# Performance work log

Measured on AMD Instinct MI355X. Metric: run time of the kernel, lower is better.

The kernel has to match this reference:

```python
import jax, jax.numpy as jnp
import numpy as np
from math import sqrt

THRESHOLD = 0.5
NEG_POS_RATIO = 3
ALPHA = 1.0


def make_priors():
    fms = [(38, 0.1, [1.0, 2.0, 0.5]), (19, 0.2, [1.0, 2.0, 0.5, 3.0, 1.0 / 3]),
           (10, 0.375, [1.0, 2.0, 0.5, 3.0, 1.0 / 3]), (5, 0.55, [1.0, 2.0, 0.5, 3.0, 1.0 / 3]),
           (3, 0.725, [1.0, 2.0, 0.5]), (1, 0.9, [1.0, 2.0, 0.5])]
    scales = [0.1, 0.2, 0.375, 0.55, 0.725, 0.9]
    priors = []
    for k, (d, s, ratios) in enumerate(fms):
        for i in range(d):
            for j in range(d):
                cx = (i + 0.5) / d
                cy = (j + 0.5) / d
                for r in ratios:
                    priors.append([cx, cy, s * sqrt(r), s / sqrt(r)])
                    if r == 1.0:
                        add = sqrt(scales[k] * scales[k + 1]) if k + 1 < len(scales) else 1.0
                        priors.append([cx, cy, add, add])
    return np.clip(np.asarray(priors, dtype=np.float32), 0.0, 1.0)  # [8732, 4]


def cxcy_to_xy(b):
    return jnp.concatenate([b[..., :2] - b[..., 2:] / 2.0, b[..., :2] + b[..., 2:] / 2.0], -1)


def jaccard(a, b):
    # a: [O,4] cxcy, b: [P,4] cxcy -> IoU [O,P]
    a_xy, b_xy = cxcy_to_xy(a), cxcy_to_xy(b)
    lt = jnp.maximum(a_xy[:, None, :2], b_xy[None, :, :2])
    rb = jnp.minimum(a_xy[:, None, 2:], b_xy[None, :, 2:])
    wh = jnp.clip(rb - lt, 0.0)
    inter = wh[..., 0] * wh[..., 1]
    area_a = (a_xy[:, 2] - a_xy[:, 0]) * (a_xy[:, 3] - a_xy[:, 1])
    area_b = (b_xy[:, 2] - b_xy[:, 0]) * (b_xy[:, 3] - b_xy[:, 1])
    return inter / (area_a[:, None] + area_b[None, :] - inter)


def cxcy_to_gcxgcy(cxcy, priors):
    g_cxcy = (cxcy[..., :2] - priors[..., :2]) / (priors[..., 2:] / 10.0)
    g_wh = jnp.log(cxcy[..., 2:] / priors[..., 2:]) * 5.0
    return jnp.concatenate([g_cxcy, g_wh], -1)


def match_one(boxes_i, priors):
    # boxes_i: [O,4] cxcy
    n_obj = boxes_i.shape[0]
    ov = jaccard(boxes_i, priors)                      # [O, P]
    ov_per_prior = ov.max(0)                           # [P]
    obj_per_prior = ov.argmax(0)                       # [P]
    prior_per_obj = ov.argmax(1)                       # [O]
    obj_per_prior = obj_per_prior.at[prior_per_obj].set(jnp.arange(n_obj))
    ov_per_prior = ov_per_prior.at[prior_per_obj].set(1.0)
    labels = (ov_per_prior >= THRESHOLD).astype(jnp.int32)  # [P], 1=text 0=bg
    true_locs = cxcy_to_gcxgcy(boxes_i[obj_per_prior], priors)  # [P,4]
    return labels, true_locs


def setup_inputs() -> dict:
    key = jax.random.key(0)
    k1, k2, k3, k4 = jax.random.split(key, 4)
    priors = jnp.asarray(make_priors())
    B, P, O = 512, priors.shape[0], 16
    predicted_locs = jax.random.normal(k1, (B, P, 4), dtype=jnp.float32)
    predicted_scores = jax.random.normal(k2, (B, P, 2), dtype=jnp.float32)
    centers = 0.2 + 0.6 * jax.random.uniform(k3, (B, O, 2), dtype=jnp.float32)
    wh = 0.05 + 0.35 * jax.random.uniform(k4, (B, O, 2), dtype=jnp.float32)
    boxes = jnp.concatenate([centers, wh], -1)  # cxcy format
    return {"predicted_locs": predicted_locs, "predicted_scores": predicted_scores,
            "boxes": boxes, "priors": priors}


def reference(predicted_locs, predicted_scores, boxes, priors):
    B, P, _ = predicted_locs.shape
    labels, true_locs = jax.vmap(match_one, in_axes=(0, None))(boxes, priors)  # [B,P], [B,P,4]
    pos = labels != 0
    mask = pos.astype(predicted_locs.dtype)            # [B,P]
    n_pos = pos.sum(1)                                 # [B]

    # localization L1 loss (mean over positive box coordinates)
    loc_abs = jnp.abs(predicted_locs - true_locs).sum(-1)  # [B,P]
    loc_loss = (loc_abs * mask).sum() / (mask.sum() * 4.0)

    # per-prior cross-entropy
    logp = jax.nn.log_softmax(predicted_scores, -1)
    ce = -jnp.take_along_axis(logp, labels[..., None], -1)[..., 0]  # [B,P]

    conf_pos = (ce * mask).sum()
    ce_neg = jnp.where(pos, 0.0, ce)
    ce_neg = jnp.sort(ce_neg, axis=1)[:, ::-1]         # descending
    hard = jnp.arange(P)[None, :] < (NEG_POS_RATIO * n_pos)[:, None]
    conf_hn = (ce_neg * hard.astype(ce_neg.dtype)).sum()
    conf_loss = (conf_pos + conf_hn) / n_pos.sum().astype(predicted_locs.dtype)
    return conf_loss + ALPHA * loc_loss
```

## Files before the change

kernel.cpp:

```cpp
#include <hip/hip_runtime.h>

#define NP 8732
#define NQ (NP / 4)
#define NPT 35
#define NO 16
#define BLK 256
#define NWAVE (BLK / 64)
#define SPLIT 4
#define CHUNK (NP / SPLIT)


__global__ __launch_bounds__(BLK, 8) void match_kernel(
    const float* __restrict__ boxes,
    const float* __restrict__ priors,
    unsigned char* __restrict__ g_obj,
    float* __restrict__ g_bv,
    int*   __restrict__ g_bi)
{
    const int b    = blockIdx.x;
    const int s    = blockIdx.y;
    const int tid  = threadIdx.x;
    const int lane = tid & 63;
    const int wv   = tid >> 6;
    const int quad = tid & 3;
    const int objLo = quad << 2;
    const int lo = s * CHUNK, hi = lo + CHUNK;

    __shared__ float s_bxy[NO][4];
    __shared__ float s_barea[NO];
    __shared__ float s_redv[NO * NWAVE];
    __shared__ int   s_redi[NO * NWAVE];

    if (tid < NO) {
        const float* bx = boxes + (size_t)b * NO * 4 + tid * 4;
        float cx = bx[0], cy = bx[1], w = bx[2], h = bx[3];
        s_bxy[tid][0] = cx - w * 0.5f; s_bxy[tid][1] = cy - h * 0.5f;
        s_bxy[tid][2] = cx + w * 0.5f; s_bxy[tid][3] = cy + h * 0.5f;
        s_barea[tid] = w * h;
    }
    __syncthreads();

    float rx0[4], ry0[4], rx1[4], ry1[4], ra[4];
#pragma unroll
    for (int j = 0; j < 4; j++) {
        rx0[j] = s_bxy[objLo + j][0]; ry0[j] = s_bxy[objLo + j][1];
        rx1[j] = s_bxy[objLo + j][2]; ry1[j] = s_bxy[objLo + j][3];
        ra[j]  = s_barea[objLo + j];
    }

    float tbv[4]; int tbp[4];
#pragma unroll
    for (int j = 0; j < 4; j++) { tbv[j] = -1.0f; tbp[j] = lo; }

    unsigned char* obj_row = g_obj + (size_t)b * NP;
    for (int p = lo + (tid >> 2); p < hi; p += (BLK / 4)) {
        float4 pr = ((const float4*)priors)[p];
        float px0 = pr.x - pr.z * 0.5f, py0 = pr.y - pr.w * 0.5f;
        float px1 = pr.x + pr.z * 0.5f, py1 = pr.y + pr.w * 0.5f;
        float areab = pr.z * pr.w;
        float bv = -1.0f; int bo = objLo;
#pragma unroll
        for (int j = 0; j < 4; j++) {
            float ix0 = fmaxf(rx0[j], px0);
            float iy0 = fmaxf(ry0[j], py0);
            float ix1 = fminf(rx1[j], px1);
            float iy1 = fminf(ry1[j], py1);
            float iw = fmaxf(ix1 - ix0, 0.0f);
            float ih = fmaxf(iy1 - iy0, 0.0f);
            float inter = iw * ih;
            float den = ra[j] + areab - inter;
            float iou = inter * __builtin_amdgcn_rcpf(den);
            if (iou > bv)     { bv = iou; bo = objLo + j; }
            if (iou > tbv[j]) { tbv[j] = iou; tbp[j] = p; }
        }
        float vN = __shfl_xor(bv, 1, 64);
        int   oN = __shfl_xor(bo, 1, 64);
        bool take = (quad & 1) ? (vN >= bv) : (vN > bv);
        if (take) { bv = vN; bo = oN; }
        vN = __shfl_xor(bv, 2, 64);
        oN = __shfl_xor(bo, 2, 64);
        take = (quad & 2) ? (vN >= bv) : (vN > bv);
        if (take) { bv = vN; bo = oN; }
        if (quad == 0) {
            bool pos = (bv >= 0.5f);
            obj_row[p] = (unsigned char)(bo | (pos ? 0x80 : 0));
        }
    }

#pragma unroll
    for (int j = 0; j < 4; j++) {
        float v = tbv[j]; int i = tbp[j];
        for (int off = 32; off >= 4; off >>= 1) {
            float v2 = __shfl_down(v, off, 64);
            int   i2 = __shfl_down(i, off, 64);
            if (v2 > v || (v2 == v && i2 < i)) { v = v2; i = i2; }
        }
        if (lane < 4) {
            s_redv[(objLo + j) * NWAVE + wv] = v;
            s_redi[(objLo + j) * NWAVE + wv] = i;
        }
    }
    __syncthreads();
    if (tid < NO) {
        float v = s_redv[tid * NWAVE]; int i = s_redi[tid * NWAVE];
#pragma unroll
        for (int w = 1; w < NWAVE; w++) {
            float v2 = s_redv[tid * NWAVE + w]; int i2 = s_redi[tid * NWAVE + w];
            if (v2 > v || (v2 == v && i2 < i)) { v = v2; i = i2; }
        }
        g_bv[((size_t)b * NO + tid) * SPLIT + s] = v;
        g_bi[((size_t)b * NO + tid) * SPLIT + s] = i;
    }
}

__device__ __forceinline__ int hist_select(unsigned* hist, unsigned* s_part,
                                           unsigned* s_csuf, unsigned* s_sel,
                                           unsigned& kk, int tid, int lane, int wv)
{
    unsigned ps = 0;
#pragma unroll
    for (int i = 0; i < 16; i++) ps += hist[tid * 16 + i];
    s_part[tid] = ps;
    __syncthreads();
    if (wv == 0) {
        unsigned c0 = s_part[4 * lane + 0], c1 = s_part[4 * lane + 1];
        unsigned c2 = s_part[4 * lane + 2], c3 = s_part[4 * lane + 3];
        unsigned g = c0 + c1 + c2 + c3;
        unsigned incl = g;
#pragma unroll
        for (int off = 1; off < 64; off <<= 1) {
            unsigned o = __shfl_down(incl, off, 64);
            if (lane + off < 64) incl += o;
        }
        unsigned excl = incl - g;
        s_csuf[4 * lane + 3] = excl;
        s_csuf[4 * lane + 2] = excl + c3;
        s_csuf[4 * lane + 1] = excl + c3 + c2;
        s_csuf[4 * lane + 0] = excl + c3 + c2 + c1;
    }
    __syncthreads();
    unsigned base = s_csuf[tid];
    if (base < kk && kk <= base + s_part[tid]) {
        unsigned run = base;
        for (int i = 15; i >= 0; i--) {
            unsigned h = hist[tid * 16 + i];
            if (kk <= run + h) { s_sel[0] = (unsigned)(tid * 16 + i); s_sel[1] = kk - run; break; }
            run += h;
        }
    }
    __syncthreads();
    kk = s_sel[1];
    return (int)s_sel[0];
}

__global__ __launch_bounds__(BLK, 2) void loss_kernel(
    const float* __restrict__ plocs,
    const float* __restrict__ pscores,
    const float* __restrict__ boxes,
    const float* __restrict__ priors,
    const unsigned char* __restrict__ g_obj,
    const float* __restrict__ g_bv,
    const int*   __restrict__ g_bi,
    float* __restrict__ loc_out,
    float* __restrict__ conf_out,
    int*   __restrict__ npos_out)
{
    const int b    = blockIdx.x;
    const int tid  = threadIdx.x;
    const int lane = tid & 63;
    const int wv   = tid >> 6;

    __shared__ unsigned char s_obj[NP];
    __shared__ unsigned s_hist[4096];
    __shared__ unsigned s_part[256];
    __shared__ unsigned s_csuf[256];
    __shared__ unsigned s_sel[2];
    __shared__ float s_bcw[NO][4];
    __shared__ int   s_bestp[NO];
    __shared__ float s_tval;
    __shared__ float s_fred[3 * NWAVE];
    __shared__ int   s_ired[NWAVE];

    const unsigned* objw = (const unsigned*)(g_obj + (size_t)b * NP);
    for (int i = tid; i < NP / 4; i += BLK) ((unsigned*)s_obj)[i] = objw[i];
    if (tid < NO * 4) ((float*)s_bcw)[tid] = boxes[(size_t)b * NO * 4 + tid];
    if (tid < NO) {
        const float* bv = g_bv + ((size_t)b * NO + tid) * SPLIT;
        const int*   bi = g_bi + ((size_t)b * NO + tid) * SPLIT;
        float v = bv[0]; int i = bi[0];
#pragma unroll
        for (int s = 1; s < SPLIT; s++) {
            float v2 = bv[s]; int i2 = bi[s];
            if (v2 > v || (v2 == v && i2 < i)) { v = v2; i = i2; }
        }
        s_bestp[tid] = i;
    }
    __syncthreads();
    if (tid == 0) {
#pragma unroll
        for (int o = 0; o < NO; o++) s_obj[s_bestp[o]] = (unsigned char)(0x80 | o);
    }
    __syncthreads();

    float ce[NPT];
    float loc_sum = 0.0f, conf_pos = 0.0f; int np = 0;
    const float2* sc2 = (const float2*)(pscores + (size_t)b * NP * 2);
    const float4* pl4 = (const float4*)(plocs  + (size_t)b * NP * 4);
#pragma unroll
    for (int k = 0; k < NPT; k++) {
        int p = tid + k * BLK;
        float v = 0.0f;
        if (p < NP) {
            unsigned m = s_obj[p];
            bool pos = (m & 0x80) != 0;
            float2 s = sc2[p];
            float mx = fmaxf(s.x, s.y);
            float dd = fabsf(s.x - s.y);
            float cev = mx + __logf(1.0f + __expf(-dd)) - (pos ? s.y : s.x);
            if (pos) {
                np++;
                conf_pos += cev;
                int o = m & 15;
                float4 pr = ((const float4*)priors)[p];
                float gx = (s_bcw[o][0] - pr.x) / (pr.z / 10.0f);
                float gy = (s_bcw[o][1] - pr.y) / (pr.w / 10.0f);
                float gw = __logf(s_bcw[o][2] / pr.z) * 5.0f;
                float gh = __logf(s_bcw[o][3] / pr.w) * 5.0f;
                float4 pl = pl4[p];
                loc_sum += fabsf(pl.x - gx) + fabsf(pl.y - gy)
                         + fabsf(pl.z - gw) + fabsf(pl.w - gh);
            } else {
                v = cev;
            }
        }
        ce[k] = v;
    }

    int npw = np;
    for (int off = 32; off; off >>= 1) npw += __shfl_down(npw, off, 64);
    if (lane == 0) s_ired[wv] = npw;
    __syncthreads();
    int n_pos = 0;
#pragma unroll
    for (int w = 0; w < NWAVE; w++) n_pos += s_ired[w];

    const int K = 3 * n_pos;
    const bool selAll = (K >= NP);
    float t = 0.0f;
    if (!selAll) {
        unsigned kk = (unsigned)K;
        for (int i = tid; i < 4096; i += BLK) s_hist[i] = 0u;
        __syncthreads();
#pragma unroll
        for (int k = 0; k < NPT; k++)
            atomicAdd(&s_hist[__float_as_uint(ce[k]) >> 19], 1u);
        __syncthreads();
        unsigned b1 = (unsigned)hist_select(s_hist, s_part, s_csuf, s_sel, kk, tid, lane, wv);
        unsigned cnt1 = s_hist[b1];
        if (cnt1 == 1u) {
#pragma unroll
            for (int k = 0; k < NPT; k++)
                if ((__float_as_uint(ce[k]) >> 19) == b1) s_tval = ce[k];
            __syncthreads();
            t = s_tval;
        } else {
            __syncthreads();
            for (int i = tid; i < 4096; i += BLK) s_hist[i] = 0u;
            __syncthreads();
#pragma unroll
            for (int k = 0; k < NPT; k++) {
                unsigned u = __float_as_uint(ce[k]);
                if ((u >> 19) == b1) atomicAdd(&s_hist[(u >> 7) & 0xFFFu], 1u);
            }
            __syncthreads();
            unsigned b2 = (unsigned)hist_select(s_hist, s_part, s_csuf, s_sel, kk, tid, lane, wv);
            unsigned p2 = (b1 << 12) | b2;
            unsigned cnt2 = s_hist[b2];
            if (cnt2 == 1u) {
#pragma unroll
                for (int k = 0; k < NPT; k++)
                    if ((__float_as_uint(ce[k]) >> 7) == p2) s_tval = ce[k];
                __syncthreads();
                t = s_tval;
            } else {
                __syncthreads();
                for (int i = tid; i < 4096; i += BLK) s_hist[i] = 0u;
                __syncthreads();
#pragma unroll
                for (int k = 0; k < NPT; k++) {
                    unsigned u = __float_as_uint(ce[k]);
                    if ((u >> 7) == p2) atomicAdd(&s_hist[u & 0x7Fu], 1u);
                }
                __syncthreads();
                unsigned b3 = (unsigned)hist_select(s_hist, s_part, s_csuf, s_sel, kk, tid, lane, wv);
                t = __uint_as_float((p2 << 7) | b3);
            }
        }
    }

    float sgt = 0.0f; int cgt = 0;
#pragma unroll
    for (int k = 0; k < NPT; k++) {
        float v = ce[k];
        if (selAll || v > t) { sgt += v; cgt++; }
    }

    float a = sgt, c = conf_pos, l = loc_sum; int g = cgt;
    for (int off = 32; off; off >>= 1) {
        a += __shfl_down(a, off, 64);
        c += __shfl_down(c, off, 64);
        l += __shfl_down(l, off, 64);
        g += __shfl_down(g, off, 64);
    }
    __syncthreads();
    if (lane == 0) {
        s_fred[wv] = a; s_fred[NWAVE + wv] = c; s_fred[2 * NWAVE + wv] = l;
        s_ired[wv] = g;
    }
    __syncthreads();
    if (tid == 0) {
        float sa = 0.0f, sc = 0.0f, sl = 0.0f; int sg = 0;
#pragma unroll
        for (int w = 0; w < NWAVE; w++) {
            sa += s_fred[w]; sc += s_fred[NWAVE + w]; sl += s_fred[2 * NWAVE + w];
            sg += s_ired[w];
        }
        float conf_hn = selAll ? sa : (sa + (float)(K - sg) * t);
        conf_out[b] = sc + conf_hn;
        loc_out[b]  = sl;
        npos_out[b] = n_pos;
    }
}

__global__ __launch_bounds__(BLK, 2) void mbox_row_kernel(
    const float* __restrict__ plocs, const float* __restrict__ pscores,
    const float* __restrict__ boxes, const float* __restrict__ priors,
    float* __restrict__ loc_out, float* __restrict__ conf_out,
    int* __restrict__ npos_out)
{
    const int b = blockIdx.x, tid = threadIdx.x, lane = tid & 63, wv = tid >> 6;
    const int par = tid & 1, objLo = par << 3;
    __shared__ __align__(16) float s_ce[NP];
    __shared__ unsigned char s_obj[NP];
    __shared__ float s_bcw[NO][4], s_bxy[NO][4], s_barea[NO];
    __shared__ float s_redv[NO * NWAVE]; __shared__ int s_redi[NO * NWAVE];
    __shared__ int s_bestp[NO];
    __shared__ unsigned s_hist16[16];
    __shared__ float s_tval;
    __shared__ float s_fred[3 * NWAVE]; __shared__ int s_ired[NWAVE];

    if (tid < NO * 4) ((float*)s_bcw)[tid] = boxes[(size_t)b * NO * 4 + tid];
    __syncthreads();
    if (tid < NO) {
        float cx = s_bcw[tid][0], cy = s_bcw[tid][1], w = s_bcw[tid][2], h = s_bcw[tid][3];
        s_bxy[tid][0] = cx - w * 0.5f; s_bxy[tid][1] = cy - h * 0.5f;
        s_bxy[tid][2] = cx + w * 0.5f; s_bxy[tid][3] = cy + h * 0.5f;
        s_barea[tid] = w * h;
    }
    __syncthreads();
    float rx0[8], ry0[8], rx1[8], ry1[8], ra[8];
#pragma unroll
    for (int j = 0; j < 8; j++) {
        rx0[j] = s_bxy[objLo + j][0]; ry0[j] = s_bxy[objLo + j][1];
        rx1[j] = s_bxy[objLo + j][2]; ry1[j] = s_bxy[objLo + j][3];
        ra[j]  = s_barea[objLo + j];
    }
    float tbv[8]; int tbp[8];
#pragma unroll
    for (int j = 0; j < 8; j++) { tbv[j] = -1.0f; tbp[j] = 0; }
    for (int p = (tid >> 1); p < NP; p += (BLK / 2)) {
        float4 pr = ((const float4*)priors)[p];
        float px0 = pr.x - pr.z * 0.5f, py0 = pr.y - pr.w * 0.5f;
        float px1 = pr.x + pr.z * 0.5f, py1 = pr.y + pr.w * 0.5f;
        float areab = pr.z * pr.w;
        float bv = -1.0f; int bo = objLo;
#pragma unroll
        for (int j = 0; j < 8; j++) {
            float ix0 = fmaxf(rx0[j], px0), iy0 = fmaxf(ry0[j], py0);
            float ix1 = fminf(rx1[j], px1), iy1 = fminf(ry1[j], py1);
            float iw = fmaxf(ix1 - ix0, 0.0f), ih = fmaxf(iy1 - iy0, 0.0f);
            float inter = iw * ih, den = ra[j] + areab - inter;
            float iou = inter * __builtin_amdgcn_rcpf(den);
            if (iou > bv) { bv = iou; bo = objLo + j; }
            if (iou > tbv[j]) { tbv[j] = iou; tbp[j] = p; }
        }
        float vN = __shfl_xor(bv, 1, 64); int oN = __shfl_xor(bo, 1, 64);
        bool take = par ? (vN >= bv) : (vN > bv);
        if (take) { bv = vN; bo = oN; }
        if (par == 0) s_obj[p] = (unsigned char)(bo | ((bv >= 0.5f) ? 0x80 : 0));
    }
#pragma unroll
    for (int j = 0; j < 8; j++) {
        float v = tbv[j]; int i = tbp[j];
        for (int off = 32; off >= 2; off >>= 1) {
            float v2 = __shfl_down(v, off, 64); int i2 = __shfl_down(i, off, 64);
            if (v2 > v || (v2 == v && i2 < i)) { v = v2; i = i2; }
        }
        if (lane < 2) { s_redv[(objLo + j) * NWAVE + wv] = v; s_redi[(objLo + j) * NWAVE + wv] = i; }
    }
    __syncthreads();
    if (tid < NO) {
        float v = s_redv[tid * NWAVE]; int i = s_redi[tid * NWAVE];
#pragma unroll
        for (int w = 1; w < NWAVE; w++) {
            float v2 = s_redv[tid * NWAVE + w]; int i2 = s_redi[tid * NWAVE + w];
            if (v2 > v || (v2 == v && i2 < i)) { v = v2; i = i2; }
        }
        s_bestp[tid] = i;
    }
    __syncthreads();
    if (tid == 0) {
#pragma unroll
        for (int o = 0; o < NO; o++) s_obj[s_bestp[o]] = (unsigned char)(0x80 | o);
    }
    __syncthreads();
    float loc_sum = 0.0f, conf_pos = 0.0f; int np = 0;
    const float2* sc2 = (const float2*)(pscores + (size_t)b * NP * 2);
    const float4* pl4 = (const float4*)(plocs + (size_t)b * NP * 4);
    for (int p = tid; p < NP; p += BLK) {
        unsigned m = s_obj[p]; bool pos = (m & 0x80) != 0;
        float2 s = sc2[p];
        float mx = fmaxf(s.x, s.y), dd = fabsf(s.x - s.y);
        float cev = mx + __logf(1.0f + __expf(-dd)) - (pos ? s.y : s.x);
        if (pos) {
            np++; conf_pos += cev;
            int o = m & 15;
            float4 pr = ((const float4*)priors)[p];
            float gx = (s_bcw[o][0] - pr.x) / (pr.z / 10.0f);
            float gy = (s_bcw[o][1] - pr.y) / (pr.w / 10.0f);
            float gw = __logf(s_bcw[o][2] / pr.z) * 5.0f;
            float gh = __logf(s_bcw[o][3] / pr.w) * 5.0f;
            float4 pl = pl4[p];
            loc_sum += fabsf(pl.x - gx) + fabsf(pl.y - gy) + fabsf(pl.z - gw) + fabsf(pl.w - gh);
            s_ce[p] = 0.0f;
        } else s_ce[p] = cev;
    }
    int npw = np;
    for (int off = 32; off; off >>= 1) npw += __shfl_down(npw, off, 64);
    if (lane == 0) s_ired[wv] = npw;
    __syncthreads();
    int n_pos = 0;
#pragma unroll
    for (int w = 0; w < NWAVE; w++) n_pos += s_ired[w];
    const int K = 3 * n_pos; const bool selAll = (K >= NP);
    float t = 0.0f;
    const float4* ce4 = (const float4*)s_ce;
    if (!selAll) {
        unsigned prefix = 0u, kk = (unsigned)K; bool done = false;
        for (int shift = 28; shift >= 0 && !done; shift -= 4) {
            __syncthreads();
            if (tid < 16) s_hist16[tid] = 0u;
            __syncthreads();
            unsigned maskhi = (shift == 28) ? 0u : (0xFFFFFFFFu << (shift + 4));
            for (int q = tid; q < NQ; q += BLK) {
                float4 v = ce4[q];
#pragma unroll
                for (int j = 0; j < 4; j++) {
                    unsigned u = __float_as_uint(j == 0 ? v.x : j == 1 ? v.y : j == 2 ? v.z : v.w);
                    if ((u & maskhi) == prefix) atomicAdd(&s_hist16[(u >> shift) & 15u], 1u);
                }
            }
            __syncthreads();
            int dsel = 15; unsigned cnt;
            for (;; dsel--) { cnt = s_hist16[dsel]; if (kk <= cnt || dsel == 0) break; kk -= cnt; }
            prefix |= ((unsigned)dsel << shift);
            if (shift > 0 && cnt == 1u) {
                unsigned mh = 0xFFFFFFFFu << shift;
                for (int q = tid; q < NQ; q += BLK) {
                    float4 v = ce4[q];
#pragma unroll
                    for (int j = 0; j < 4; j++) {
                        float f = (j == 0 ? v.x : j == 1 ? v.y : j == 2 ? v.z : v.w);
                        if ((__float_as_uint(f) & mh) == prefix) s_tval = f;
                    }
                }
                __syncthreads();
                t = s_tval; done = true;
            } else if (shift == 0) t = __uint_as_float(prefix);
        }
    }
    float sgt = 0.0f; int cgt = 0;
    for (int q = tid; q < NQ; q += BLK) {
        float4 v = ce4[q];
        if (selAll || v.x > t) { sgt += v.x; cgt++; }
        if (selAll || v.y > t) { sgt += v.y; cgt++; }
        if (selAll || v.z > t) { sgt += v.z; cgt++; }
        if (selAll || v.w > t) { sgt += v.w; cgt++; }
    }
    float a = sgt, c = conf_pos, l = loc_sum; int g = cgt;
    for (int off = 32; off; off >>= 1) {
        a += __shfl_down(a, off, 64); c += __shfl_down(c, off, 64);
        l += __shfl_down(l, off, 64); g += __shfl_down(g, off, 64);
    }
    __syncthreads();
    if (lane == 0) { s_fred[wv] = a; s_fred[NWAVE + wv] = c; s_fred[2 * NWAVE + wv] = l; s_ired[wv] = g; }
    __syncthreads();
    if (tid == 0) {
        float sa = 0, sc = 0, sl = 0; int sg = 0;
#pragma unroll
        for (int w = 0; w < NWAVE; w++) { sa += s_fred[w]; sc += s_fred[NWAVE + w]; sl += s_fred[2 * NWAVE + w]; sg += s_ired[w]; }
        float conf_hn = selAll ? sa : (sa + (float)(K - sg) * t);
        conf_out[b] = sc + conf_hn; loc_out[b] = sl; npos_out[b] = n_pos;
    }
}

__global__ __launch_bounds__(256) void mbox_finalize_kernel(
    const float* __restrict__ loc_in, const float* __restrict__ conf_in,
    const int* __restrict__ npos_in, int B, float* __restrict__ out)
{
    __shared__ float sl[4], sc[4];
    __shared__ int si[4];
    int tid = threadIdx.x, lane = tid & 63, wv = tid >> 6;
    float l = 0.0f, c = 0.0f; int n = 0;
    for (int i = tid; i < B; i += 256) { l += loc_in[i]; c += conf_in[i]; n += npos_in[i]; }
    for (int off = 32; off; off >>= 1) {
        l += __shfl_down(l, off, 64);
        c += __shfl_down(c, off, 64);
        n += __shfl_down(n, off, 64);
    }
    if (lane == 0) { sl[wv] = l; sc[wv] = c; si[wv] = n; }
    __syncthreads();
    if (tid == 0) {
        float tl = sl[0] + sl[1] + sl[2] + sl[3];
        float tc = sc[0] + sc[1] + sc[2] + sc[3];
        int tn = si[0] + si[1] + si[2] + si[3];
        float fn = (float)tn;
        out[0] = tc / fn + tl / (fn * 4.0f);
    }
}

extern "C" void kernel_launch(void* const* d_in, const int* in_sizes, int n_in,
                              void* d_out, int out_size, void* d_ws, size_t ws_size,
                              hipStream_t stream) {
    const float* plocs   = (const float*)d_in[0];
    const float* pscores = (const float*)d_in[1];
    const float* boxes   = (const float*)d_in[2];
    const float* priors  = (const float*)d_in[3];
    const int B = in_sizes[0] / (NP * 4);

    float* loc_ws  = (float*)d_ws;
    float* conf_ws = loc_ws + B;
    int*   np_ws   = (int*)(conf_ws + B);
    float* g_bv    = (float*)(np_ws + B);
    int*   g_bi    = (int*)(g_bv + (size_t)B * NO * SPLIT);
    unsigned char* g_obj = (unsigned char*)(g_bi + (size_t)B * NO * SPLIT);
    size_t need = (size_t)(3 * B) * 4 + (size_t)B * NO * SPLIT * 8 + (size_t)B * NP;

    if (ws_size >= need) {
        match_kernel<<<dim3(B, SPLIT), BLK, 0, stream>>>(boxes, priors, g_obj, g_bv, g_bi);
        loss_kernel<<<B, BLK, 0, stream>>>(plocs, pscores, boxes, priors,
                                           g_obj, g_bv, g_bi, loc_ws, conf_ws, np_ws);
    } else {
        mbox_row_kernel<<<B, BLK, 0, stream>>>(plocs, pscores, boxes, priors,
                                               loc_ws, conf_ws, np_ws);
    }
    mbox_finalize_kernel<<<1, 256, 0, stream>>>(loc_ws, conf_ws, np_ws, B, (float*)d_out);
}
```

Measured before the change: 196.6 us.

## Split per-row loss into parallel CE kernel and candidate-based select kernel

Replaces the one-block-per-batch-row loss kernel with a ce_kernel that runs SPLIT blocks per row. Each block writes per-prior negative CE to global memory and merges its coarse histogram into a global per-row histogram with atomics. A separate select_kernel reads that histogram to find the threshold bin, gathers the candidates in that bin into shared memory, and refines the top-k threshold there instead of re-scanning the whole row several times. This spreads the CE work across more blocks, at the cost of extra launches (including a histogram-zeroing kernel), a global CE round trip, and global atomics.

```diff
diff --git a/kernel.cpp b/kernel.cpp
--- a/kernel.cpp
+++ b/kernel.cpp
@@ -2,15 +2,15 @@
 
 #define NP 8732
 #define NQ (NP / 4)
-#define NPT 35
 #define NO 16
 #define BLK 256
 #define NWAVE (BLK / 64)
 #define SPLIT 4
 #define CHUNK (NP / SPLIT)
-
-
-__global__ __launch_bounds__(BLK, 8) void match_kernel(
+#define CAP 4096
+
+
+__global__ __launch_bounds__(BLK, 4) void match_kernel(
     const float* __restrict__ boxes,
     const float* __restrict__ priors,
     unsigned char* __restrict__ g_obj,
@@ -113,47 +113,12 @@
     }
 }
 
-__device__ __forceinline__ int hist_select(unsigned* hist, unsigned* s_part,
-                                           unsigned* s_csuf, unsigned* s_sel,
-                                           unsigned& kk, int tid, int lane, int wv)
-{
-    unsigned ps = 0;
-#pragma unroll
-    for (int i = 0; i < 16; i++) ps += hist[tid * 16 + i];
-    s_part[tid] = ps;
-    __syncthreads();
-    if (wv == 0) {
-        unsigned c0 = s_part[4 * lane + 0], c1 = s_part[4 * lane + 1];
-        unsigned c2 = s_part[4 * lane + 2], c3 = s_part[4 * lane + 3];
-        unsigned g = c0 + c1 + c2 + c3;
-        unsigned incl = g;
-#pragma unroll
-        for (int off = 1; off < 64; off <<= 1) {
-            unsigned o = __shfl_down(incl, off, 64);
-            if (lane + off < 64) incl += o;
-        }
-        unsigned excl = incl - g;
-        s_csuf[4 * lane + 3] = excl;
-        s_csuf[4 * lane + 2] = excl + c3;
-        s_csuf[4 * lane + 1] = excl + c3 + c2;
-        s_csuf[4 * lane + 0] = excl + c3 + c2 + c1;
-    }
-    __syncthreads();
-    unsigned base = s_csuf[tid];
-    if (base < kk && kk <= base + s_part[tid]) {
-        unsigned run = base;
-        for (int i = 15; i >= 0; i--) {
-            unsigned h = hist[tid * 16 + i];
-            if (kk <= run + h) { s_sel[0] = (unsigned)(tid * 16 + i); s_sel[1] = kk - run; break; }
-            run += h;
-        }
-    }
-    __syncthreads();
-    kk = s_sel[1];
-    return (int)s_sel[0];
-}
-
-__global__ __launch_bounds__(BLK, 2) void loss_kernel(
+__global__ __launch_bounds__(BLK) void zero_hist_kernel(uint4* g, int n4) {
+    int i = blockIdx.x * BLK + threadIdx.x;
+    if (i < n4) g[i] = make_uint4(0u, 0u, 0u, 0u);
+}
+
+__global__ __launch_bounds__(BLK, 4) void ce_kernel(
     const float* __restrict__ plocs,
     const float* __restrict__ pscores,
     const float* __restrict__ boxes,
@@ -161,62 +126,64 @@
     const unsigned char* __restrict__ g_obj,
     const float* __restrict__ g_bv,
     const int*   __restrict__ g_bi,
-    float* __restrict__ loc_out,
-    float* __restrict__ conf_out,
-    int*   __restrict__ npos_out)
+    float* __restrict__ g_ce,
+    unsigned* __restrict__ g_hist,
+    float* __restrict__ g_part)
 {
     const int b    = blockIdx.x;
+    const int s    = blockIdx.y;
     const int tid  = threadIdx.x;
     const int lane = tid & 63;
     const int wv   = tid >> 6;
-
-    __shared__ unsigned char s_obj[NP];
-    __shared__ unsigned s_hist[4096];
-    __shared__ unsigned s_part[256];
-    __shared__ unsigned s_csuf[256];
-    __shared__ unsigned s_sel[2];
+    const int lo = s * CHUNK, hi = lo + CHUNK;
+
+    __shared__ unsigned char s_objc[CHUNK];
     __shared__ float s_bcw[NO][4];
     __shared__ int   s_bestp[NO];
-    __shared__ float s_tval;
-    __shared__ float s_fred[3 * NWAVE];
-    __shared__ int   s_ired[NWAVE];
-
-    const unsigned* objw = (const unsigned*)(g_obj + (size_t)b * NP);
-    for (int i = tid; i < NP / 4; i += BLK) ((unsigned*)s_obj)[i] = objw[i];
+    __shared__ unsigned s_hist[4096];
+    __shared__ float s_f[3 * NWAVE];
+    __shared__ int   s_i[NWAVE];
+
+    const unsigned char* obj_row = g_obj + (size_t)b * NP;
+    for (int i = tid; i < CHUNK; i += BLK) s_objc[i] = obj_row[lo + i];
     if (tid < NO * 4) ((float*)s_bcw)[tid] = boxes[(size_t)b * NO * 4 + tid];
     if (tid < NO) {
         const float* bv = g_bv + ((size_t)b * NO + tid) * SPLIT;
         const int*   bi = g_bi + ((size_t)b * NO + tid) * SPLIT;
         float v = bv[0]; int i = bi[0];
 #pragma unroll
-        for (int s = 1; s < SPLIT; s++) {
-            float v2 = bv[s]; int i2 = bi[s];
+        for (int k = 1; k < SPLIT; k++) {
+            float v2 = bv[k]; int i2 = bi[k];
             if (v2 > v || (v2 == v && i2 < i)) { v = v2; i = i2; }
         }
         s_bestp[tid] = i;
     }
+    for (int i = tid; i < 4096; i += BLK) s_hist[i] = 0u;
     __syncthreads();
     if (tid == 0) {
 #pragma unroll
-        for (int o = 0; o < NO; o++) s_obj[s_bestp[o]] = (unsigned char)(0x80 | o);
-    }
-    __syncthreads();
-
-    float ce[NPT];
-    float loc_sum = 0.0f, conf_pos = 0.0f; int np = 0;
+        for (int o = 0; o < NO; o++) {
+            int bp = s_bestp[o];
+            if (bp >= lo && bp < hi) s_objc[bp - lo] = (unsigned char)(0x80 | o);
+        }
+    }
+    __syncthreads();
+
+    float loc_sum = 0.0f, conf_pos = 0.0f, ce_sum = 0.0f; int np = 0;
     const float2* sc2 = (const float2*)(pscores + (size_t)b * NP * 2);
     const float4* pl4 = (const float4*)(plocs  + (size_t)b * NP * 4);
-#pragma unroll
-    for (int k = 0; k < NPT; k++) {
-        int p = tid + k * BLK;
-        float v = 0.0f;
-        if (p < NP) {
-            unsigned m = s_obj[p];
+    float* ce_row = g_ce + (size_t)b * NP;
+#pragma unroll
+    for (int k = 0; k < 9; k++) {
+        int p = lo + tid + k * BLK;
+        if (p < hi) {
+            unsigned m = s_objc[p - lo];
             bool pos = (m & 0x80) != 0;
-            float2 s = sc2[p];
-            float mx = fmaxf(s.x, s.y);
-            float dd = fabsf(s.x - s.y);
-            float cev = mx + __logf(1.0f + __expf(-dd)) - (pos ? s.y : s.x);
+            float2 sv = sc2[p];
+            float mx = fmaxf(sv.x, sv.y);
+            float dd = fabsf(sv.x - sv.y);
+            float cev = mx + __logf(1.0f + __expf(-dd)) - (pos ? sv.y : sv.x);
+            float v = 0.0f;
             if (pos) {
                 np++;
                 conf_pos += cev;
@@ -232,178 +199,281 @@
             } else {
                 v = cev;
             }
-        }
-        ce[k] = v;
-    }
-
-    int npw = np;
-    for (int off = 32; off; off >>= 1) npw += __shfl_down(npw, off, 64);
-    if (lane == 0) s_ired[wv] = npw;
-    __syncthreads();
-    int n_pos = 0;
-#pragma unroll
-    for (int w = 0; w < NWAVE; w++) n_pos += s_ired[w];
-
-    const int K = 3 * n_pos;
-    const bool selAll = (K >= NP);
-    float t = 0.0f;
-    if (!selAll) {
-        unsigned kk = (unsigned)K;
-        for (int i = tid; i < 4096; i += BLK) s_hist[i] = 0u;
-        __syncthreads();
-#pragma unroll
-        for (int k = 0; k < NPT; k++)
-            atomicAdd(&s_hist[__float_as_uint(ce[k]) >> 19], 1u);
-        __syncthreads();
-        unsigned b1 = (unsigned)hist_select(s_hist, s_part, s_csuf, s_sel, kk, tid, lane, wv);
-        unsigned cnt1 = s_hist[b1];
-        if (cnt1 == 1u) {
-#pragma unroll
-            for (int k = 0; k < NPT; k++)
-                if ((__float_as_uint(ce[k]) >> 19) == b1) s_tval = ce[k];
-            __syncthreads();
-            t = s_tval;
-        } else {
-            __syncthreads();
-            for (int i = tid; i < 4096; i += BLK) s_hist[i] = 0u;
-            __syncthreads();
-#pragma unroll
-            for (int k = 0; k < NPT; k++) {
-                unsigned u = __float_as_uint(ce[k]);
-                if ((u >> 19) == b1) atomicAdd(&s_hist[(u >> 7) & 0xFFFu], 1u);
-            }
-            __syncthreads();
-            unsigned b2 = (unsigned)hist_select(s_hist, s_part, s_csuf, s_sel, kk, tid, lane, wv);
-            unsigned p2 = (b1 << 12) | b2;
-            unsigned cnt2 = s_hist[b2];
-            if (cnt2 == 1u) {
-#pragma unroll
-                for (int k = 0; k < NPT; k++)
-                    if ((__float_as_uint(ce[k]) >> 7) == p2) s_tval = ce[k];
-                __syncthreads();
-                t = s_tval;
-            } else {
-                __syncthreads();
-                for (int i = tid; i < 4096; i += BLK) s_hist[i] = 0u;
-                __syncthreads();
-#pragma unroll
-                for (int k = 0; k < NPT; k++) {
-                    unsigned u = __float_as_uint(ce[k]);
-                    if ((u >> 7) == p2) atomicAdd(&s_hist[u & 0x7Fu], 1u);
-                }
-                __syncthreads();
-                unsigned b3 = (unsigned)hist_select(s_hist, s_part, s_csuf, s_sel, kk, tid, lane, wv);
-                t = __uint_as_float((p2 << 7) | b3);
-            }
-        }
-    }
-
-    float sgt = 0.0f; int cgt = 0;
-#pragma unroll
-    for (int k = 0; k < NPT; k++) {
-        float v = ce[k];
-        if (selAll || v > t) { sgt += v; cgt++; }
-    }
-
-    float a = sgt, c = conf_pos, l = loc_sum; int g = cgt;
+            ce_row[p] = v;
+            ce_sum += v;
+            atomicAdd(&s_hist[__float_as_uint(v) >> 19], 1u);
+        }
+    }
+    __syncthreads();
+
+    unsigned* gh = g_hist + (size_t)b * 4096;
+    for (int i = tid; i < 4096; i += BLK) {
+        unsigned h = s_hist[i];
+        if (h) atomicAdd(&gh[i], h);
+    }
+
+    float a = (float)np, c = conf_pos, l = loc_sum, e = ce_sum;
     for (int off = 32; off; off >>= 1) {
         a += __shfl_down(a, off, 64);
         c += __shfl_down(c, off, 64);
         l += __shfl_down(l, off, 64);
-        g += __shfl_down(g, off, 64);
-    }
-    __syncthreads();
-    if (lane == 0) {
-        s_fred[wv] = a; s_fred[NWAVE + wv] = c; s_fred[2 * NWAVE + wv] = l;
-        s_ired[wv] = g;
-    }
+        e += __shfl_down(e, off, 64);
+    }
+    if (lane == 0) { s_f[wv] = a; s_f[NWAVE + wv] = c; s_f[2 * NWAVE + wv] = l; s_i[wv] = __float_as_int(e); }
     __syncthreads();
     if (tid == 0) {
-        float sa = 0.0f, sc = 0.0f, sl = 0.0f; int sg = 0;
+        float sa = 0, sc = 0, sl = 0, se = 0;
 #pragma unroll
         for (int w = 0; w < NWAVE; w++) {
-            sa += s_fred[w]; sc += s_fred[NWAVE + w]; sl += s_fred[2 * NWAVE + w];
-            sg += s_ired[w];
-        }
-        float conf_hn = selAll ? sa : (sa + (float)(K - sg) * t);
-        conf_out[b] = sc + conf_hn;
-        loc_out[b]  = sl;
+            sa += s_f[w]; sc += s_f[NWAVE + w]; sl += s_f[2 * NWAVE + w];
+            se += __int_as_float(s_i[w]);
+        }
+        float* pp = g_part + ((size_t)b * SPLIT + s) * 4;
+        pp[0] = sa; pp[1] = sc; pp[2] = sl; pp[3] = se;
+    }
+}
+
+__device__ __forceinline__ int hist_select(unsigned* hist, unsigned* s_part,
+                                           unsigned* s_csuf, unsigned* s_sel,
+                                           unsigned& kk, int tid, int lane, int wv)
+{
+    unsigned ps = 0;
+#pragma unroll
+    for (int i = 0; i < 16; i++) ps += hist[tid * 16 + i];
+    s_part[tid] = ps;
+    __syncthreads();
+    if (wv == 0) {
+        unsigned c0 = s_part[4 * lane + 0], c1 = s_part[4 * lane + 1];
+        unsigned c2 = s_part[4 * lane + 2], c3 = s_part[4 * lane + 3];
+        unsigned g = c0 + c1 + c2 + c3;
+        unsigned incl = g;
+#pragma unroll
+        for (int off = 1; off < 64; off <<= 1) {
+            unsigned o = __shfl_down(incl, off, 64);
+            if (lane + off < 64) incl += o;
+        }
+        unsigned excl = incl - g;
+        s_csuf[4 * lane + 3] = excl;
+        s_csuf[4 * lane + 2] = excl + c3;
+        s_csuf[4 * lane + 1] = excl + c3 + c2;
+        s_csuf[4 * lane + 0] = excl + c3 + c2 + c1;
+    }
+    __syncthreads();
+    unsigned base = s_csuf[tid];
+    if (base < kk && kk <= base + s_part[tid]) {
+        unsigned run = base;
+        for (int i = 15; i >= 0; i--) {
+            unsigned h = hist[tid * 16 + i];
+            if (kk <= run + h) { s_sel[0] = (unsigned)(tid * 16 + i); s_sel[1] = kk - run; break; }
+            run += h;
+        }
+    }
+    __syncthreads();
+    kk = s_sel[1];
+    return (int)s_sel[0];
+}
+
+__global__ __launch_bounds__(BLK, 2) void select_kernel(
+    const float* __restrict__ g_ce,
+    const unsigned* __restrict__ g_hist,
+    const float* __restrict__ g_part,
+    float* __restrict__ loc_out,
+    float* __restrict__ conf_out,
+    int*   __restrict__ npos_out)
+{
+    const int b    = blockIdx.x;
+    const int tid  = threadIdx.x;
+    const int lane = tid & 63;
+    const int wv   = tid >> 6;
+
+    __shared__ unsigned s_hist[4096];
+    __shared__ float    s_cand[CAP];
+    __shared__ unsigned s_part[256];
+    __shared__ unsigned s_csuf[256];
+    __shared__ unsigned s_sel[2];
+    __shared__ unsigned s_cnt;
+    __shared__ float    s_tval;
+    __shared__ float    s_f[NWAVE];
+    __shared__ int      s_i[NWAVE];
+
+    float npf = 0, cp = 0, loc = 0, cs = 0;
+#pragma unroll
+    for (int k = 0; k < SPLIT; k++) {
+        const float* pp = g_part + ((size_t)b * SPLIT + k) * 4;
+        npf += pp[0]; cp += pp[1]; loc += pp[2]; cs += pp[3];
+    }
+    const int n_pos = (int)(npf + 0.5f);
+    const int K = 3 * n_pos;
+
+    if (K >= NP) {
+        if (tid == 0) { conf_out[b] = cp + cs; loc_out[b] = loc; npos_out[b] = n_pos; }
+        return;
+    }
+
+    const unsigned* gh = g_hist + (size_t)b * 4096;
+    for (int i = tid; i < 4096; i += BLK) s_hist[i] = gh[i];
+    if (tid == 0) s_cnt = 0u;
+    __syncthreads();
+
+    unsigned kk = (unsigned)K;
+    unsigned b1 = (unsigned)hist_select(s_hist, s_part, s_csuf, s_sel, kk, tid, lane, wv);
+    const unsigned kk_bin = kk;
+    const unsigned m_total = s_hist[b1];
+
+    const float4* row = (const float4*)(g_ce + (size_t)b * NP);
+    float shi = 0.0f;
+    for (int q = tid; q < NQ; q += BLK) {
+        float4 v = row[q];
+#pragma unroll
+        for (int j = 0; j < 4; j++) {
+            float f = (j == 0 ? v.x : j == 1 ? v.y : j == 2 ? v.z : v.w);
+            unsigned bin = __float_as_uint(f) >> 19;
+            if (bin > b1) shi += f;
+            else if (bin == b1) {
+                unsigned idx = atomicAdd(&s_cnt, 1u);
+                if (idx < CAP) s_cand[idx] = f;
+            }
+        }
+    }
+    for (int off = 32; off; off >>= 1) shi += __shfl_down(shi, off, 64);
+    if (lane == 0) s_f[wv] = shi;
+    __syncthreads();
+    shi = 0.0f;
+#pragma unroll
+    for (int w = 0; w < NWAVE; w++) shi += s_f[w];
+
+    float conf_hn;
+    if (m_total <= (unsigned)CAP) {
+        unsigned prefix = b1 << 19;
+        float t = 0.0f;
+        bool done = false;
+        for (int shift = 16; shift >= 0 && !done; shift -= 4) {
+            __syncthreads();
+            if (tid < 16) s_part[tid] = 0u;
+            __syncthreads();
+            unsigned mh = 0xFFFFFFFFu << (shift + 4);
+            for (int i = tid; i < (int)m_total; i += BLK) {
+                unsigned u = __float_as_uint(s_cand[i]);
+                if (((u ^ prefix) & mh) == 0u)
+                    atomicAdd(&s_part[(u >> shift) & 15u], 1u);
+            }
+            __syncthreads();
+            int dsel = 15; unsigned cnt;
+            for (;; dsel--) { cnt = s_part[dsel]; if (kk <= cnt || dsel == 0) break; kk -= cnt; }
+            prefix |= ((unsigned)dsel << shift);
+            if (shift > 0 && cnt == 1u) {
+                unsigned mh2 = 0xFFFFFFFFu << shift;
+                for (int i = tid; i < (int)m_total; i += BLK) {
+                    unsigned u = __float_as_uint(s_cand[i]);
+                    if (((u ^ prefix) & mh2) == 0u) s_tval = s_cand[i];
+                }
+                __syncthreads();
+                t = s_tval; done = true;
+            } else if (shift == 0) {
+                t = __uint_as_float(prefix);
+            }
+        }
+        float sg = 0.0f; int cg = 0;
+        for (int i = tid; i < (int)m_total; i += BLK) {
+            float c = s_cand[i];
+            if (c > t) { sg += c; cg++; }
+        }
+        for (int off = 32; off; off >>= 1) {
+            sg += __shfl_down(sg, off, 64);
+            cg += __shfl_down(cg, off, 64);
+        }
+        __syncthreads();
+        if (lane == 0) { s_f[wv] = sg; s_i[wv] = cg; }
+        __syncthreads();
+        sg = 0.0f; cg = 0;
+#pragma unroll
+        for (int w = 0; w < NWAVE; w++) { sg += s_f[w]; cg += s_i[w]; }
+        conf_hn = shi + sg + (float)((int)kk_bin - cg) * t;
+    } else {
+        __syncthreads();
+        for (int i = tid; i < 4096; i += BLK) s_hist[i] = 0u;
+        __syncthreads();
+        for (int q = tid; q < NQ; q += BLK) {
+            float4 v = row[q];
+#pragma unroll
+            for (int j = 0; j < 4; j++) {
+                unsigned u = __float_as_uint(j == 0 ? v.x : j == 1 ? v.y : j == 2 ? v.z : v.w);
+                if ((u >> 19) == b1) atomicAdd(&s_hist[(u >> 7) & 0xFFFu], 1u);
+            }
+        }
+        __syncthreads();
+        unsigned b2 = (unsigned)hist_select(s_hist, s_part, s_csuf, s_sel, kk, tid, lane, wv);
+        unsigned p2 = (b1 << 12) | b2;
+        __syncthreads();
+        for (int i = tid; i < 4096; i += BLK) s_hist[i] = 0u;
+        __syncthreads();
+        for (int q = tid; q < NQ; q += BLK) {
+            float4 v = row[q];
+#pragma unroll
+            for (int j = 0; j < 4; j++) {
+                unsigned u = __float_as_uint(j == 0 ? v.x : j == 1 ? v.y : j == 2 ? v.z : v.w);
+                if ((u >> 7) == p2) atomicAdd(&s_hist[u & 0x7Fu], 1u);
+            }
+        }
+        __syncthreads();
+        unsigned b3 = (unsigned)hist_select(s_hist, s_part, s_csuf, s_sel, kk, tid, lane, wv);
+        float t = __uint_as_float((p2 << 7) | b3);
+        float sg = 0.0f; int cg = 0;
+        for (int q = tid; q < NQ; q += BLK) {
+            float4 v = row[q];
+            if (v.x > t) { sg += v.x; cg++; }
+            if (v.y > t) { sg += v.y; cg++; }
+            if (v.z > t) { sg += v.z; cg++; }
+            if (v.w > t) { sg += v.w; cg++; }
+        }
+        for (int off = 32; off; off >>= 1) {
+            sg += __shfl_down(sg, off, 64);
+            cg += __shfl_down(cg, off, 64);
+        }
+        __syncthreads();
+        if (lane == 0) { s_f[wv] = sg; s_i[wv] = cg; }
+        __syncthreads();
+        sg = 0.0f; cg = 0;
+#pragma unroll
+        for (int w = 0; w < NWAVE; w++) { sg += s_f[w]; cg += s_i[w]; }
+        conf_hn = sg + (float)(K - cg) * t;
+    }
+
+    if (tid == 0) {
+        conf_out[b] = cp + conf_hn;
+        loc_out[b]  = loc;
         npos_out[b] = n_pos;
     }
 }
 
-__global__ __launch_bounds__(BLK, 2) void mbox_row_kernel(
+__global__ __launch_bounds__(BLK, 2) void loss_kernel(
     const float* __restrict__ plocs, const float* __restrict__ pscores,
     const float* __restrict__ boxes, const float* __restrict__ priors,
+    const unsigned char* __restrict__ g_obj,
+    const float* __restrict__ g_bv, const int* __restrict__ g_bi,
     float* __restrict__ loc_out, float* __restrict__ conf_out,
     int* __restrict__ npos_out)
 {
     const int b = blockIdx.x, tid = threadIdx.x, lane = tid & 63, wv = tid >> 6;
-    const int par = tid & 1, objLo = par << 3;
     __shared__ __align__(16) float s_ce[NP];
     __shared__ unsigned char s_obj[NP];
-    __shared__ float s_bcw[NO][4], s_bxy[NO][4], s_barea[NO];
-    __shared__ float s_redv[NO * NWAVE]; __shared__ int s_redi[NO * NWAVE];
+    __shared__ unsigned s_hist[4096];
+    __shared__ unsigned s_part[256], s_csuf[256], s_sel[2];
+    __shared__ float s_bcw[NO][4];
     __shared__ int s_bestp[NO];
-    __shared__ unsigned s_hist16[16];
     __shared__ float s_tval;
     __shared__ float s_fred[3 * NWAVE]; __shared__ int s_ired[NWAVE];
 
+    const unsigned* objw = (const unsigned*)(g_obj + (size_t)b * NP);
+    for (int i = tid; i < NP / 4; i += BLK) ((unsigned*)s_obj)[i] = objw[i];
     if (tid < NO * 4) ((float*)s_bcw)[tid] = boxes[(size_t)b * NO * 4 + tid];
-    __syncthreads();
     if (tid < NO) {
-        float cx = s_bcw[tid][0], cy = s_bcw[tid][1], w = s_bcw[tid][2], h = s_bcw[tid][3];
-        s_bxy[tid][0] = cx - w * 0.5f; s_bxy[tid][1] = cy - h * 0.5f;
-        s_bxy[tid][2] = cx + w * 0.5f; s_bxy[tid][3] = cy + h * 0.5f;
-        s_barea[tid] = w * h;
-    }
-    __syncthreads();
-    float rx0[8], ry0[8], rx1[8], ry1[8], ra[8];
-#pragma unroll
-    for (int j = 0; j < 8; j++) {
-        rx0[j] = s_bxy[objLo + j][0]; ry0[j] = s_bxy[objLo + j][1];
-        rx1[j] = s_bxy[objLo + j][2]; ry1[j] = s_bxy[objLo + j][3];
-        ra[j]  = s_barea[objLo + j];
-    }
-    float tbv[8]; int tbp[8];
-#pragma unroll
-    for (int j = 0; j < 8; j++) { tbv[j] = -1.0f; tbp[j] = 0; }
-    for (int p = (tid >> 1); p < NP; p += (BLK / 2)) {
-        float4 pr = ((const float4*)priors)[p];
-        float px0 = pr.x - pr.z * 0.5f, py0 = pr.y - pr.w * 0.5f;
-        float px1 = pr.x + pr.z * 0.5f, py1 = pr.y + pr.w * 0.5f;
-        float areab = pr.z * pr.w;
-        float bv = -1.0f; int bo = objLo;
-#pragma unroll
-        for (int j = 0; j < 8; j++) {
-            float ix0 = fmaxf(rx0[j], px0), iy0 = fmaxf(ry0[j], py0);
-            float ix1 = fminf(rx1[j], px1), iy1 = fminf(ry1[j], py1);
-            float iw = fmaxf(ix1 - ix0, 0.0f), ih = fmaxf(iy1 - iy0, 0.0f);
-            float inter = iw * ih, den = ra[j] + areab - inter;
-            float iou = inter * __builtin_amdgcn_rcpf(den);
-            if (iou > bv) { bv = iou; bo = objLo + j; }
-            if (iou > tbv[j]) { tbv[j] = iou; tbp[j] = p; }
-        }
-        float vN = __shfl_xor(bv, 1, 64); int oN = __shfl_xor(bo, 1, 64);
-        bool take = par ? (vN >= bv) : (vN > bv);
-        if (take) { bv = vN; bo = oN; }
-        if (par == 0) s_obj[p] = (unsigned char)(bo | ((bv >= 0.5f) ? 0x80 : 0));
-    }
-#pragma unroll
-    for (int j = 0; j < 8; j++) {
-        float v = tbv[j]; int i = tbp[j];
-        for (int off = 32; off >= 2; off >>= 1) {
-            float v2 = __shfl_down(v, off, 64); int i2 = __shfl_down(i, off, 64);
-            if (v2 > v || (v2 == v && i2 < i)) { v = v2; i = i2; }
-        }
-        if (lane < 2) { s_redv[(objLo + j) * NWAVE + wv] = v; s_redi[(objLo + j) * NWAVE + wv] = i; }
-    }
-    __syncthreads();
-    if (tid < NO) {
-        float v = s_redv[tid * NWAVE]; int i = s_redi[tid * NWAVE];
-#pragma unroll
-        for (int w = 1; w < NWAVE; w++) {
-            float v2 = s_redv[tid * NWAVE + w]; int i2 = s_redi[tid * NWAVE + w];
+        const float* bv = g_bv + ((size_t)b * NO + tid) * SPLIT;
+        const int*   bi = g_bi + ((size_t)b * NO + tid) * SPLIT;
+        float v = bv[0]; int i = bi[0];
+#pragma unroll
+        for (int s = 1; s < SPLIT; s++) {
+            float v2 = bv[s]; int i2 = bi[s];
             if (v2 > v || (v2 == v && i2 < i)) { v = v2; i = i2; }
         }
         s_bestp[tid] = i;
@@ -446,38 +516,46 @@
     float t = 0.0f;
     const float4* ce4 = (const float4*)s_ce;
     if (!selAll) {
-        unsigned prefix = 0u, kk = (unsigned)K; bool done = false;
-        for (int shift = 28; shift >= 0 && !done; shift -= 4) {
-            __syncthreads();
-            if (tid < 16) s_hist16[tid] = 0u;
-            __syncthreads();
-            unsigned maskhi = (shift == 28) ? 0u : (0xFFFFFFFFu << (shift + 4));
-            for (int q = tid; q < NQ; q += BLK) {
-                float4 v = ce4[q];
-#pragma unroll
-                for (int j = 0; j < 4; j++) {
-                    unsigned u = __float_as_uint(j == 0 ? v.x : j == 1 ? v.y : j == 2 ? v.z : v.w);
-                    if ((u & maskhi) == prefix) atomicAdd(&s_hist16[(u >> shift) & 15u], 1u);
-                }
-            }
-            __syncthreads();
-            int dsel = 15; unsigned cnt;
-            for (;; dsel--) { cnt = s_hist16[dsel]; if (kk <= cnt || dsel == 0) break; kk -= cnt; }
-            prefix |= ((unsigned)dsel << shift);
-            if (shift > 0 && cnt == 1u) {
-                unsigned mh = 0xFFFFFFFFu << shift;
-                for (int q = tid; q < NQ; q += BLK) {
-                    float4 v = ce4[q];
-#pragma unroll
-                    for (int j = 0; j < 4; j++) {
-                        float f = (j == 0 ? v.x : j == 1 ? v.y : j == 2 ? v.z : v.w);
-                        if ((__float_as_uint(f) & mh) == prefix) s_tval = f;
-                    }
-                }
-                __syncthreads();
-                t = s_tval; done = true;
-            } else if (shift == 0) t = __uint_as_float(prefix);
-        }
+        unsigned kk = (unsigned)K;
+        for (int i = tid; i < 4096; i += BLK) s_hist[i] = 0u;
+        __syncthreads();
+        for (int q = tid; q < NQ; q += BLK) {
+            float4 v = ce4[q];
+            atomicAdd(&s_hist[__float_as_uint(v.x) >> 19], 1u);
+            atomicAdd(&s_hist[__float_as_uint(v.y) >> 19], 1u);
+            atomicAdd(&s_hist[__float_as_uint(v.z) >> 19], 1u);
+            atomicAdd(&s_hist[__float_as_uint(v.w) >> 19], 1u);
+        }
+        __syncthreads();
+        unsigned b1 = (unsigned)hist_select(s_hist, s_part, s_csuf, s_sel, kk, tid, lane, wv);
+        __syncthreads();
+        for (int i = tid; i < 4096; i += BLK) s_hist[i] = 0u;
+        __syncthreads();
+        for (int q = tid; q < NQ; q += BLK) {
+            float4 v = ce4[q];
+#pragma unroll
+            for (int j = 0; j < 4; j++) {
+                unsigned u = __float_as_uint(j == 0 ? v.x : j == 1 ? v.y : j == 2 ? v.z : v.w);
+                if ((u >> 19) == b1) atomicAdd(&s_hist[(u >> 7) & 0xFFFu], 1u);
+            }
+        }
+        __syncthreads();
+        unsigned b2 = (unsigned)hist_select(s_hist, s_part, s_csuf, s_sel, kk, tid, lane, wv);
+        unsigned p2 = (b1 << 12) | b2;
+        __syncthreads();
+        for (int i = tid; i < 4096; i += BLK) s_hist[i] = 0u;
+        __syncthreads();
+        for (int q = tid; q < NQ; q += BLK) {
+            float4 v = ce4[q];
+#pragma unroll
+            for (int j = 0; j < 4; j++) {
+                unsigned u = __float_as_uint(j == 0 ? v.x : j == 1 ? v.y : j == 2 ? v.z : v.w);
+                if ((u >> 7) == p2) atomicAdd(&s_hist[u & 0x7Fu], 1u);
+            }
+        }
+        __syncthreads();
+        unsigned b3 = (unsigned)hist_select(s_hist, s_part, s_csuf, s_sel, kk, tid, lane, wv);
+        t = __uint_as_float((p2 << 7) | b3);
     }
     float sgt = 0.0f; int cgt = 0;
     for (int q = tid; q < NQ; q += BLK) {
@@ -543,16 +621,28 @@
     int*   np_ws   = (int*)(conf_ws + B);
     float* g_bv    = (float*)(np_ws + B);
     int*   g_bi    = (int*)(g_bv + (size_t)B * NO * SPLIT);
-    unsigned char* g_obj = (unsigned char*)(g_bi + (size_t)B * NO * SPLIT);
-    size_t need = (size_t)(3 * B) * 4 + (size_t)B * NO * SPLIT * 8 + (size_t)B * NP;
-
-    if (ws_size >= need) {
+    float* g_part  = (float*)(g_bi + (size_t)B * NO * SPLIT);
+    unsigned* g_hist = (unsigned*)(g_part + (size_t)B * SPLIT * 4);
+    float* g_ce    = (float*)(g_hist + (size_t)B * 4096);
+    unsigned char* g_obj = (unsigned char*)(g_ce + (size_t)B * NP);
+    size_t need_full = (size_t)((char*)(g_obj + (size_t)B * NP) - (char*)d_ws);
+
+    if (ws_size >= need_full) {
+        int n4 = B * 4096 / 4;
+        zero_hist_kernel<<<(n4 + BLK - 1) / BLK, BLK, 0, stream>>>((uint4*)g_hist, n4);
         match_kernel<<<dim3(B, SPLIT), BLK, 0, stream>>>(boxes, priors, g_obj, g_bv, g_bi);
-        loss_kernel<<<B, BLK, 0, stream>>>(plocs, pscores, boxes, priors,
-                                           g_obj, g_bv, g_bi, loc_ws, conf_ws, np_ws);
+        ce_kernel<<<dim3(B, SPLIT), BLK, 0, stream>>>(plocs, pscores, boxes, priors,
+                                                      g_obj, g_bv, g_bi, g_ce, g_hist, g_part);
+        select_kernel<<<B, BLK, 0, stream>>>(g_ce, g_hist, g_part,
+                                             loc_ws, conf_ws, np_ws);
     } else {
-        mbox_row_kernel<<<B, BLK, 0, stream>>>(plocs, pscores, boxes, priors,
-                                               loc_ws, conf_ws, np_ws);
+        unsigned char* g_obj2 = (unsigned char*)(g_bi + (size_t)B * NO * SPLIT);
+        size_t need_mid = (size_t)((char*)(g_obj2 + (size_t)B * NP) - (char*)d_ws);
+        if (ws_size >= need_mid) {
+            match_kernel<<<dim3(B, SPLIT), BLK, 0, stream>>>(boxes, priors, g_obj2, g_bv, g_bi);
+            loss_kernel<<<B, BLK, 0, stream>>>(plocs, pscores, boxes, priors,
+                                               g_obj2, g_bv, g_bi, loc_ws, conf_ws, np_ws);
+        }
     }
     mbox_finalize_kernel<<<1, 256, 0, stream>>>(loc_ws, conf_ws, np_ws, B, (float*)d_out);
 }
```

Result: slower. 204.9 us (+4.2%).
